# Kernel optimization log

Measured on AMD Instinct MI355X. Metric: run time of the kernel, lower is better.

## Reference

```python
import jax, jax.numpy as jnp
import numpy as np

N_NODES = 50000


def _segment_softmax(alpha, dst, num_segments):
    # alpha: [E, H] edge attention logits, softmax-normalized per destination node
    m = jax.ops.segment_max(alpha, dst, num_segments=num_segments)
    m = jnp.where(jnp.isfinite(m), m, 0.0)
    e = jnp.exp(alpha - m[dst])
    s = jax.ops.segment_sum(e, dst, num_segments=num_segments)
    return e / (s[dst] + 1e-16)


def _gat_layer(x, W, att_src, att_dst, bias, src, dst, heads, ch, concat):
    N = x.shape[0]
    xp = (x @ W).reshape(N, heads, ch)                      # [N, H, C]
    a_s = jnp.einsum('nhc,hc->nh', xp, att_src)              # [N, H]
    a_d = jnp.einsum('nhc,hc->nh', xp, att_dst)              # [N, H]
    alpha = jax.nn.leaky_relu(a_s[src] + a_d[dst], 0.2)      # [E, H]
    alpha = _segment_softmax(alpha, dst, N)
    out = jax.ops.segment_sum(alpha[:, :, None] * xp[src], dst, num_segments=N)  # [N, H, C]
    out = out.reshape(N, heads * ch) if concat else out.mean(axis=1)
    return out + bias


def setup_inputs() -> dict:
    key = jax.random.key(0)
    ks = jax.random.split(key, 10)
    IN, HID, HEADS, OUT, E = 128, 64, 4, 32, 640000
    x = jax.random.normal(ks[0], (N_NODES, IN), jnp.float32)
    edge_index = jax.random.randint(ks[1], (2, E), 0, N_NODES, dtype=jnp.int32)
    W1 = jax.random.normal(ks[2], (IN, HEADS * HID), jnp.float32) * (1.0 / np.sqrt(IN))
    att_src1 = jax.random.normal(ks[3], (HEADS, HID), jnp.float32) * 0.1
    att_dst1 = jax.random.normal(ks[4], (HEADS, HID), jnp.float32) * 0.1
    b1 = jnp.zeros((HEADS * HID,), jnp.float32)
    W2 = jax.random.normal(ks[5], (HEADS * HID, OUT), jnp.float32) * (1.0 / np.sqrt(HEADS * HID))
    att_src2 = jax.random.normal(ks[6], (1, OUT), jnp.float32) * 0.1
    att_dst2 = jax.random.normal(ks[7], (1, OUT), jnp.float32) * 0.1
    b2 = jnp.zeros((OUT,), jnp.float32)
    return {"x": x, "edge_index": edge_index, "W1": W1, "att_src1": att_src1,
            "att_dst1": att_dst1, "b1": b1, "W2": W2, "att_src2": att_src2,
            "att_dst2": att_dst2, "b2": b2}


def reference(x, edge_index, W1, att_src1, att_dst1, b1, W2, att_src2, att_dst2, b2):
    N = x.shape[0]
    # PyG GATConv default: add self-loops
    loop = jnp.arange(N, dtype=edge_index.dtype)
    src = jnp.concatenate([edge_index[0], loop])
    dst = jnp.concatenate([edge_index[1], loop])
    HID = att_src1.shape[1]
    HEADS = att_src1.shape[0]
    OUT = att_src2.shape[1]
    # dropout layers are identity in eval mode
    h = jax.nn.elu(_gat_layer(x, W1, att_src1, att_dst1, b1, src, dst, HEADS, HID, True))
    out = _gat_layer(h, W2, att_src2, att_dst2, b2, src, dst, 1, OUT, False)
    return jax.nn.softmax(out, axis=1)
```

## Files before the change

### kernel.cpp

```cpp
#include <hip/hip_runtime.h>
#include <math.h>
#include <stdint.h>

#define NEG_SENT -1e30f

typedef __attribute__((ext_vector_type(8))) short bf16x8;
typedef __attribute__((ext_vector_type(4))) float f32x4;

__device__ __forceinline__ unsigned short f2bf(float f) {
    unsigned u = __float_as_uint(f);
    unsigned r = u + 0x7FFFu + ((u >> 16) & 1u);
    return (unsigned short)(r >> 16);
}
__device__ __forceinline__ float bf2f(unsigned short h) {
    return __uint_as_float(((unsigned)h) << 16);
}

__global__ __launch_bounds__(256) void transpose_w(const float* __restrict__ w1,
        const float* __restrict__ w2, unsigned short* __restrict__ w1t,
        unsigned short* __restrict__ w2t) {
    int tidx = blockIdx.x * 256 + threadIdx.x;
    if (blockIdx.x < 128) {
        int k = tidx & 127, n = tidx >> 7;
        w1t[tidx] = f2bf(w1[k * 256 + n]);
    } else {
        int idx = tidx - 32768;
        int k = idx & 255, n = idx >> 8;
        w2t[idx] = f2bf(w2[k * 32 + n]);
    }
}

__global__ __launch_bounds__(256) void gemm1_mfma(
        const float* __restrict__ x,
        const unsigned short* __restrict__ w1t,
        const float* __restrict__ att_s, const float* __restrict__ att_d,
        unsigned short* __restrict__ xph,
        float* __restrict__ a_s, float* __restrict__ a_d, int M) {
    int wave = (int)(((long)blockIdx.x * 256 + threadIdx.x) >> 6);
    int lane = threadIdx.x & 63;
    int row0 = wave * 16;
    if (row0 >= M) return;
    int r = lane & 15;
    int g = lane >> 4;
    bf16x8 a[4];
    const float* arow = x + (long)(row0 + r) * 128 + g * 8;
    #pragma unroll
    for (int k0 = 0; k0 < 4; ++k0) {
        float4 f0 = *(const float4*)(arow + k0 * 32);
        float4 f1 = *(const float4*)(arow + k0 * 32 + 4);
        bf16x8 af;
        af[0] = (short)f2bf(f0.x); af[1] = (short)f2bf(f0.y);
        af[2] = (short)f2bf(f0.z); af[3] = (short)f2bf(f0.w);
        af[4] = (short)f2bf(f1.x); af[5] = (short)f2bf(f1.y);
        af[6] = (short)f2bf(f1.z); af[7] = (short)f2bf(f1.w);
        a[k0] = af;
    }
    float as_v[16], ad_v[16];
    #pragma unroll
    for (int nt = 0; nt < 16; ++nt) {
        as_v[nt] = att_s[nt * 16 + r];
        ad_v[nt] = att_d[nt * 16 + r];
    }
    f32x4 acc[16];
    #pragma unroll
    for (int nt = 0; nt < 16; ++nt) acc[nt] = (f32x4){0.f, 0.f, 0.f, 0.f};
    #pragma unroll
    for (int nt = 0; nt < 16; ++nt) {
        const unsigned short* brow = w1t + (long)(nt * 16 + r) * 128 + g * 8;
        #pragma unroll
        for (int k0 = 0; k0 < 4; ++k0) {
            bf16x8 b = *(const bf16x8*)(brow + k0 * 32);
            acc[nt] = __builtin_amdgcn_mfma_f32_16x16x32_bf16(a[k0], b, acc[nt], 0, 0, 0);
        }
    }
    float ps[4][4] = {};
    float pd[4][4] = {};
    #pragma unroll
    for (int nt = 0; nt < 16; ++nt) {
        int hh = nt >> 2;
        #pragma unroll
        for (int q = 0; q < 4; ++q) {
            float v = acc[nt][q];
            xph[(long)(row0 + g * 4 + q) * 256 + nt * 16 + r] = f2bf(v);
            ps[q][hh] += v * as_v[nt];
            pd[q][hh] += v * ad_v[nt];
        }
    }
    #pragma unroll
    for (int off = 1; off < 16; off <<= 1) {
        #pragma unroll
        for (int q = 0; q < 4; ++q)
            #pragma unroll
            for (int hh = 0; hh < 4; ++hh) {
                ps[q][hh] += __shfl_xor(ps[q][hh], off);
                pd[q][hh] += __shfl_xor(pd[q][hh], off);
            }
    }
    if (r == 0) {
        #pragma unroll
        for (int q = 0; q < 4; ++q) {
            int row = row0 + g * 4 + q;
            #pragma unroll
            for (int hh = 0; hh < 4; ++hh) {
                a_s[row * 4 + hh] = ps[q][hh];
                a_d[row * 4 + hh] = pd[q][hh];
            }
        }
    }
}

__global__ __launch_bounds__(256) void gemm2_mfma(
        const unsigned short* __restrict__ hb,
        const unsigned short* __restrict__ w2t,
        const float* __restrict__ att_s, const float* __restrict__ att_d,
        unsigned short* __restrict__ xp2h,
        float* __restrict__ a_s, float* __restrict__ a_d, int M) {
    int wave = (int)(((long)blockIdx.x * 256 + threadIdx.x) >> 6);
    int lane = threadIdx.x & 63;
    int row0 = wave * 16;
    if (row0 >= M) return;
    int r = lane & 15;
    int g = lane >> 4;
    bf16x8 a[8];
    const unsigned short* arow = hb + (long)(row0 + r) * 256 + g * 8;
    #pragma unroll
    for (int k0 = 0; k0 < 8; ++k0)
        a[k0] = *(const bf16x8*)(arow + k0 * 32);
    float as_v[2], ad_v[2];
    #pragma unroll
    for (int nt = 0; nt < 2; ++nt) {
        as_v[nt] = att_s[nt * 16 + r];
        ad_v[nt] = att_d[nt * 16 + r];
    }
    f32x4 acc[2];
    acc[0] = (f32x4){0.f, 0.f, 0.f, 0.f};
    acc[1] = (f32x4){0.f, 0.f, 0.f, 0.f};
    #pragma unroll
    for (int nt = 0; nt < 2; ++nt) {
        const unsigned short* brow = w2t + (long)(nt * 16 + r) * 256 + g * 8;
        #pragma unroll
        for (int k0 = 0; k0 < 8; ++k0) {
            bf16x8 b = *(const bf16x8*)(brow + k0 * 32);
            acc[nt] = __builtin_amdgcn_mfma_f32_16x16x32_bf16(a[k0], b, acc[nt], 0, 0, 0);
        }
    }
    float ps[4] = {}, pd[4] = {};
    #pragma unroll
    for (int nt = 0; nt < 2; ++nt) {
        #pragma unroll
        for (int q = 0; q < 4; ++q) {
            float v = acc[nt][q];
            xp2h[(long)(row0 + g * 4 + q) * 32 + nt * 16 + r] = f2bf(v);
            ps[q] += v * as_v[nt];
            pd[q] += v * ad_v[nt];
        }
    }
    #pragma unroll
    for (int off = 1; off < 16; off <<= 1) {
        #pragma unroll
        for (int q = 0; q < 4; ++q) {
            ps[q] += __shfl_xor(ps[q], off);
            pd[q] += __shfl_xor(pd[q], off);
        }
    }
    if (r == 0) {
        #pragma unroll
        for (int q = 0; q < 4; ++q) {
            a_s[row0 + g * 4 + q] = ps[q];
            a_d[row0 + g * 4 + q] = pd[q];
        }
    }
}

__global__ __launch_bounds__(256) void count_deg(const int* __restrict__ ei,
        int E, int Etot, int* __restrict__ deg) {
    int e = blockIdx.x * 256 + threadIdx.x;
    if (e >= Etot) return;
    int d = (e < E) ? ei[E + e] : e - E;
    atomicAdd(&deg[d], 1);
}

__global__ __launch_bounds__(256) void scan_local(const int* __restrict__ deg,
        int* __restrict__ rowptr, int* __restrict__ blocksum, int N) {
    __shared__ int part[256];
    int b = blockIdx.x, t = threadIdx.x;
    int base = b * 1024 + t * 4;
    int4 v = make_int4(0, 0, 0, 0);
    if (base + 3 < N) {
        v = *(const int4*)(deg + base);
    } else {
        if (base + 0 < N) v.x = deg[base + 0];
        if (base + 1 < N) v.y = deg[base + 1];
        if (base + 2 < N) v.z = deg[base + 2];
        if (base + 3 < N) v.w = deg[base + 3];
    }
    part[t] = v.x + v.y + v.z + v.w;
    __syncthreads();
    #pragma unroll
    for (int off = 1; off < 256; off <<= 1) {
        int val = (t >= off) ? part[t - off] : 0;
        __syncthreads();
        part[t] += val;
        __syncthreads();
    }
    if (t == 255) blocksum[b] = part[255];
    int r0 = (t > 0) ? part[t - 1] : 0;
    int r1 = r0 + v.x;
    int r2 = r1 + v.y;
    int r3 = r2 + v.z;
    if (base + 3 < N) {
        *(int4*)(rowptr + base) = make_int4(r0, r1, r2, r3);
    } else {
        if (base + 0 < N) rowptr[base + 0] = r0;
        if (base + 1 < N) rowptr[base + 1] = r1;
        if (base + 2 < N) rowptr[base + 2] = r2;
        if (base + 3 < N) rowptr[base + 3] = r3;
    }
}

__global__ __launch_bounds__(256) void scan_add(int* __restrict__ rowptr,
        const int* __restrict__ blocksum, int* __restrict__ cursor,
        int N, int Etot, int nb) {
    __shared__ int part[256];
    int b = blockIdx.x, t = threadIdx.x;
    part[t] = (t < nb) ? blocksum[t] : 0;
    __syncthreads();
    #pragma unroll
    for (int off = 1; off < 256; off <<= 1) {
        int val = (t >= off) ? part[t - off] : 0;
        __syncthreads();
        part[t] += val;
        __syncthreads();
    }
    int off_b = (b > 0) ? part[b - 1] : 0;
    int base = b * 1024 + t * 4;
    if (base + 3 < N) {
        int4 v = *(const int4*)(rowptr + base);
        v.x += off_b; v.y += off_b; v.z += off_b; v.w += off_b;
        *(int4*)(rowptr + base) = v;
        *(int4*)(cursor + base) = v;
    } else {
        for (int i = 0; i < 4; ++i) {
            if (base + i < N) {
                int v = rowptr[base + i] + off_b;
                rowptr[base + i] = v;
                cursor[base + i] = v;
            }
        }
    }
    if (b == 0 && t == 0) rowptr[N] = Etot;
}

__global__ __launch_bounds__(256) void scatter_edges(const int* __restrict__ ei,
        int E, int Etot, int* __restrict__ cursor, int* __restrict__ csr_src) {
    int e = blockIdx.x * 256 + threadIdx.x;
    if (e >= Etot) return;
    int s, d;
    if (e < E) { s = ei[e]; d = ei[E + e]; } else { s = e - E; d = s; }
    int pos = atomicAdd(&cursor[d], 1);
    csr_src[pos] = s;
}

__global__ __launch_bounds__(256) void sort_rows(const int* __restrict__ rowptr,
        int* __restrict__ csr_src, int N) {
    __shared__ int buf[4][256];
    __shared__ int mxw[4];
    int t = threadIdx.x;
    int w = t >> 6;
    int lane = t & 63;
    int d = blockIdx.x * 4 + w;
    int row0 = 0, deg = 0;
    if (d < N) { row0 = rowptr[d]; deg = rowptr[d + 1] - row0; }
    int capped = (deg <= 256) ? deg : 0;
    for (int j = lane; j < capped; j += 64) buf[w][j] = csr_src[row0 + j];
    int m = capped;
    #pragma unroll
    for (int off = 32; off; off >>= 1) m = max(m, __shfl_xor(m, off));
    if (lane == 0) mxw[w] = m;
    __syncthreads();
    int itmax = max(max(mxw[0], mxw[1]), max(mxw[2], mxw[3]));
    for (int it = 0; it < itmax; ++it) {
        int start = it & 1;
        #pragma unroll
        for (int rep = 0; rep < 2; ++rep) {
            int k = start + 2 * lane + rep * 128;
            if (k + 1 < capped) {
                int a = buf[w][k], b = buf[w][k + 1];
                if (a > b) { buf[w][k] = b; buf[w][k + 1] = a; }
            }
        }
        __syncthreads();
    }
    for (int j = lane; j < capped; j += 64) csr_src[row0 + j] = buf[w][j];
    if (deg > 256 && lane == 0) {
        for (int i = 1; i < deg; ++i) {
            int key = csr_src[row0 + i];
            int k = i - 1;
            while (k >= 0 && csr_src[row0 + k] > key) {
                csr_src[row0 + k + 1] = csr_src[row0 + k];
                --k;
            }
            csr_src[row0 + k + 1] = key;
        }
    }
}

__device__ __forceinline__ void merge_ms(float& m, float& s, float m2, float s2) {
    float mn = fmaxf(m, m2);
    s = s * expf(m - mn) + s2 * expf(m2 - mn);
    m = mn;
}

__global__ __launch_bounds__(256) void stats_coeff_h4(const int* __restrict__ rowptr,
        const int* __restrict__ csr_src, const float* __restrict__ a_s,
        const float* __restrict__ a_d, unsigned short* __restrict__ coeff, int N) {
    int t = threadIdx.x;
    int d = blockIdx.x * 4 + (t >> 6);
    if (d >= N) return;
    int lane = t & 63;
    int h = lane & 3;
    int j0 = lane >> 2;
    int row0 = rowptr[d];
    int deg = rowptr[d + 1] - row0;
    float ad = a_d[d * 4 + h];
    float m = NEG_SENT, s = 0.f;
    for (int j = j0; j < deg; j += 16) {
        int sn = csr_src[row0 + j];
        float l = a_s[sn * 4 + h] + ad;
        l = l > 0.f ? l : 0.2f * l;
        float mn = fmaxf(m, l);
        s = s * expf(m - mn) + expf(l - mn);
        m = mn;
    }
    #pragma unroll
    for (int off = 4; off <= 32; off <<= 1) {
        float m2 = __shfl_xor(m, off);
        float s2 = __shfl_xor(s, off);
        merge_ms(m, s, m2, s2);
    }
    float inv = 1.f / (s + 1e-16f);
    for (int j = j0; j < deg; j += 16) {
        int sn = csr_src[row0 + j];
        float l = a_s[sn * 4 + h] + ad;
        l = l > 0.f ? l : 0.2f * l;
        coeff[(long)(row0 + j) * 4 + h] = f2bf(expf(l - m) * inv);
    }
}

__global__ __launch_bounds__(256) void agg1_gather_bf16(const int* __restrict__ rowptr,
        const int* __restrict__ csr_src, const unsigned short* __restrict__ coeff,
        const ushort4* __restrict__ xph4, const float* __restrict__ bias,
        ushort4* __restrict__ hb4, int N) {
    int t = threadIdx.x;
    int d = blockIdx.x * 4 + (t >> 6);
    if (d >= N) return;
    int lane = t & 63;
    int hsel = lane >> 4;
    int row0 = rowptr[d];
    int deg = rowptr[d + 1] - row0;
    float4 acc = make_float4(0.f, 0.f, 0.f, 0.f);
    int j = 0;
    for (; j + 4 <= deg; j += 4) {
        long e0 = row0 + j;
        int s0 = csr_src[e0 + 0];
        int s1 = csr_src[e0 + 1];
        int s2 = csr_src[e0 + 2];
        int s3 = csr_src[e0 + 3];
        float c0 = bf2f(coeff[(e0 + 0) * 4 + hsel]);
        float c1 = bf2f(coeff[(e0 + 1) * 4 + hsel]);
        float c2 = bf2f(coeff[(e0 + 2) * 4 + hsel]);
        float c3 = bf2f(coeff[(e0 + 3) * 4 + hsel]);
        ushort4 u0 = xph4[(long)s0 * 64 + lane];
        ushort4 u1 = xph4[(long)s1 * 64 + lane];
        ushort4 u2 = xph4[(long)s2 * 64 + lane];
        ushort4 u3 = xph4[(long)s3 * 64 + lane];
        acc.x += c0 * bf2f(u0.x); acc.y += c0 * bf2f(u0.y);
        acc.z += c0 * bf2f(u0.z); acc.w += c0 * bf2f(u0.w);
        acc.x += c1 * bf2f(u1.x); acc.y += c1 * bf2f(u1.y);
        acc.z += c1 * bf2f(u1.z); acc.w += c1 * bf2f(u1.w);
        acc.x += c2 * bf2f(u2.x); acc.y += c2 * bf2f(u2.y);
        acc.z += c2 * bf2f(u2.z); acc.w += c2 * bf2f(u2.w);
        acc.x += c3 * bf2f(u3.x); acc.y += c3 * bf2f(u3.y);
        acc.z += c3 * bf2f(u3.z); acc.w += c3 * bf2f(u3.w);
    }
    for (; j < deg; ++j) {
        long e = row0 + j;
        int s = csr_src[e];
        float c = bf2f(coeff[e * 4 + hsel]);
        ushort4 u = xph4[(long)s * 64 + lane];
        acc.x += c * bf2f(u.x); acc.y += c * bf2f(u.y);
        acc.z += c * bf2f(u.z); acc.w += c * bf2f(u.w);
    }
    float4 b = ((const float4*)bias)[lane];
    float vx = acc.x + b.x; vx = vx > 0.f ? vx : expm1f(vx);
    float vy = acc.y + b.y; vy = vy > 0.f ? vy : expm1f(vy);
    float vz = acc.z + b.z; vz = vz > 0.f ? vz : expm1f(vz);
    float vw = acc.w + b.w; vw = vw > 0.f ? vw : expm1f(vw);
    ushort4 o;
    o.x = f2bf(vx); o.y = f2bf(vy); o.z = f2bf(vz); o.w = f2bf(vw);
    hb4[(long)d * 64 + lane] = o;
}

__global__ __launch_bounds__(256) void agg2_fused(const int* __restrict__ rowptr,
        const int* __restrict__ csr_src, const float* __restrict__ a_s,
        const float* __restrict__ a_d, const unsigned short* __restrict__ xp2h,
        const float* __restrict__ bias, float* __restrict__ out, int N) {
    int t = threadIdx.x;
    int d = blockIdx.x * 8 + (t >> 5);
    if (d >= N) return;
    int c = t & 31;
    int row0 = rowptr[d];
    int deg = rowptr[d + 1] - row0;
    float ad = a_d[d];
    float m = NEG_SENT, s = 0.f;
    for (int j = c; j < deg; j += 32) {
        int sn = csr_src[row0 + j];
        float l = a_s[sn] + ad;
        l = l > 0.f ? l : 0.2f * l;
        float mn = fmaxf(m, l);
        s = s * expf(m - mn) + expf(l - mn);
        m = mn;
    }
    #pragma unroll
    for (int off = 1; off <= 16; off <<= 1) {
        float m2 = __shfl_xor(m, off, 32);
        float s2 = __shfl_xor(s, off, 32);
        merge_ms(m, s, m2, s2);
    }
    float inv = 1.f / (s + 1e-16f);
    float acc = 0.f;
    int j = 0;
    for (; j + 4 <= deg; j += 4) {
        long e0 = row0 + j;
        int s0 = csr_src[e0 + 0];
        int s1 = csr_src[e0 + 1];
        int s2 = csr_src[e0 + 2];
        int s3 = csr_src[e0 + 3];
        float l0 = a_s[s0] + ad; l0 = l0 > 0.f ? l0 : 0.2f * l0;
        float l1 = a_s[s1] + ad; l1 = l1 > 0.f ? l1 : 0.2f * l1;
        float l2 = a_s[s2] + ad; l2 = l2 > 0.f ? l2 : 0.2f * l2;
        float l3 = a_s[s3] + ad; l3 = l3 > 0.f ? l3 : 0.2f * l3;
        float c0 = expf(l0 - m) * inv;
        float c1 = expf(l1 - m) * inv;
        float c2 = expf(l2 - m) * inv;
        float c3 = expf(l3 - m) * inv;
        float v0 = bf2f(xp2h[(long)s0 * 32 + c]);
        float v1 = bf2f(xp2h[(long)s1 * 32 + c]);
        float v2 = bf2f(xp2h[(long)s2 * 32 + c]);
        float v3 = bf2f(xp2h[(long)s3 * 32 + c]);
        acc += c0 * v0;
        acc += c1 * v1;
        acc += c2 * v2;
        acc += c3 * v3;
    }
    for (; j < deg; ++j) {
        long e = row0 + j;
        int sn = csr_src[e];
        float l = a_s[sn] + ad; l = l > 0.f ? l : 0.2f * l;
        float co = expf(l - m) * inv;
        acc += co * bf2f(xp2h[(long)sn * 32 + c]);
    }
    float v = acc + bias[c];
    float mx = v;
    #pragma unroll
    for (int off = 16; off; off >>= 1) mx = fmaxf(mx, __shfl_xor(mx, off, 32));
    float ex = expf(v - mx);
    float sm = ex;
    #pragma unroll
    for (int off = 16; off; off >>= 1) sm += __shfl_xor(sm, off, 32);
    out[(long)d * 32 + c] = ex / sm;
}

extern "C" void kernel_launch(void* const* d_in, const int* in_sizes, int n_in,
                              void* d_out, int out_size, void* d_ws, size_t ws_size,
                              hipStream_t stream) {
    const float* x   = (const float*)d_in[0];
    const int*   ei  = (const int*)d_in[1];
    const float* W1  = (const float*)d_in[2];
    const float* as1 = (const float*)d_in[3];
    const float* ad1 = (const float*)d_in[4];
    const float* b1  = (const float*)d_in[5];
    const float* W2  = (const float*)d_in[6];
    const float* as2 = (const float*)d_in[7];
    const float* ad2 = (const float*)d_in[8];
    const float* b2  = (const float*)d_in[9];
    float* out = (float*)d_out;

    const int N = in_sizes[0] / 128;
    const int E = in_sizes[1] / 2;
    const int Etot = E + N;

    unsigned short* xp1h = (unsigned short*)d_ws;
    unsigned short* hb   = xp1h + (long)N * 256;
    unsigned short* w1t  = hb + (long)N * 256;
    unsigned short* w2t  = w1t + 32768;
    unsigned short* xp2h = w2t + 8192;
    float* a_s1   = (float*)(xp2h + (long)N * 32);
    float* a_d1   = a_s1 + (long)N * 4;
    float* a_s2   = a_d1 + (long)N * 4;
    float* a_d2   = a_s2 + N;
    unsigned short* coeff1 = (unsigned short*)(a_d2 + N);
    int* deg      = (int*)(coeff1 + (long)Etot * 4);
    int* rowptr   = deg + N;
    int* cursor   = rowptr + N + 4;
    int* csr_src  = cursor + N;
    int* blocksum = csr_src + Etot;

    hipMemsetAsync(deg, 0, (size_t)N * sizeof(int), stream);

    int nbE = (Etot + 255) / 256;
    int nbS = (N + 1023) / 1024;
    count_deg<<<nbE, 256, 0, stream>>>(ei, E, Etot, deg);
    scan_local<<<nbS, 256, 0, stream>>>(deg, rowptr, blocksum, N);
    scan_add<<<nbS, 256, 0, stream>>>(rowptr, blocksum, cursor, N, Etot, nbS);
    scatter_edges<<<nbE, 256, 0, stream>>>(ei, E, Etot, cursor, csr_src);
    sort_rows<<<(N + 3) / 4, 256, 0, stream>>>(rowptr, csr_src, N);

    int gemmBlocks = (((N + 15) / 16) + 3) / 4;
    transpose_w<<<160, 256, 0, stream>>>(W1, W2, w1t, w2t);

    gemm1_mfma<<<gemmBlocks, 256, 0, stream>>>(x, w1t, as1, ad1,
                                               xp1h, a_s1, a_d1, N);
    stats_coeff_h4<<<(N + 3) / 4, 256, 0, stream>>>(rowptr, csr_src, a_s1, a_d1,
                                                    coeff1, N);
    agg1_gather_bf16<<<(N + 3) / 4, 256, 0, stream>>>(rowptr, csr_src, coeff1,
                                              (const ushort4*)xp1h, b1,
                                              (ushort4*)hb, N);

    gemm2_mfma<<<gemmBlocks, 256, 0, stream>>>(hb, w2t, as2, ad2,
                                               xp2h, a_s2, a_d2, N);
    agg2_fused<<<(N + 7) / 8, 256, 0, stream>>>(rowptr, csr_src, a_s2, a_d2,
                                                xp2h, b2, out, N);
}
```

Baseline: 274.2 us.

## Fuse softmax stats with layer-1 aggregation via LDS coefficients; merge weight prep into degree count

Merges the layer-1 softmax-statistics kernel and the gather-aggregation kernel into one. Per-edge attention coefficients for up to 256 edges per node are staged in shared memory rather than written to and re-read from a global coeff buffer. Edges past 256 have their coefficient recomputed inline. The weight transpose/bf16 conversion is also folded into the degree-count kernel as extra blocks, removing one launch. The trade-off is a block-wide sync that couples four waves and 8KB of LDS per block, which may reduce occupancy.

After: 258.3 us. -5.8%, faster.

```diff
diff --git a/kernel.cpp b/kernel.cpp
--- a/kernel.cpp
+++ b/kernel.cpp
@@ -16,17 +16,26 @@
     return __uint_as_float(((unsigned)h) << 16);
 }
 
-__global__ __launch_bounds__(256) void transpose_w(const float* __restrict__ w1,
+__global__ __launch_bounds__(256) void prep_count(const float* __restrict__ w1,
         const float* __restrict__ w2, unsigned short* __restrict__ w1t,
-        unsigned short* __restrict__ w2t) {
-    int tidx = blockIdx.x * 256 + threadIdx.x;
-    if (blockIdx.x < 128) {
-        int k = tidx & 127, n = tidx >> 7;
-        w1t[tidx] = f2bf(w1[k * 256 + n]);
+        unsigned short* __restrict__ w2t, const int* __restrict__ ei,
+        int E, int Etot, int* __restrict__ deg) {
+    int b = blockIdx.x;
+    if (b < 160) {
+        int tidx = b * 256 + threadIdx.x;
+        if (b < 128) {
+            int k = tidx & 127, n = tidx >> 7;
+            w1t[tidx] = f2bf(w1[k * 256 + n]);
+        } else {
+            int idx = tidx - 32768;
+            int k = idx & 255, n = idx >> 8;
+            w2t[idx] = f2bf(w2[k * 32 + n]);
+        }
     } else {
-        int idx = tidx - 32768;
-        int k = idx & 255, n = idx >> 8;
-        w2t[idx] = f2bf(w2[k * 32 + n]);
+        int e = (b - 160) * 256 + threadIdx.x;
+        if (e >= Etot) return;
+        int d = (e < E) ? ei[E + e] : e - E;
+        atomicAdd(&deg[d], 1);
     }
 }
 
@@ -172,14 +181,6 @@
     }
 }
 
-__global__ __launch_bounds__(256) void count_deg(const int* __restrict__ ei,
-        int E, int Etot, int* __restrict__ deg) {
-    int e = blockIdx.x * 256 + threadIdx.x;
-    if (e >= Etot) return;
-    int d = (e < E) ? ei[E + e] : e - E;
-    atomicAdd(&deg[d], 1);
-}
-
 __global__ __launch_bounds__(256) void scan_local(const int* __restrict__ deg,
         int* __restrict__ rowptr, int* __restrict__ blocksum, int N) {
     __shared__ int part[256];
@@ -311,18 +312,21 @@
     m = mn;
 }
 
-__global__ __launch_bounds__(256) void stats_coeff_h4(const int* __restrict__ rowptr,
+__global__ __launch_bounds__(256) void agg1_fused(const int* __restrict__ rowptr,
         const int* __restrict__ csr_src, const float* __restrict__ a_s,
-        const float* __restrict__ a_d, unsigned short* __restrict__ coeff, int N) {
+        const float* __restrict__ a_d, const ushort4* __restrict__ xph4,
+        const float* __restrict__ bias, ushort4* __restrict__ hb4, int N) {
+    __shared__ unsigned short cbuf[4][1024];
     int t = threadIdx.x;
-    int d = blockIdx.x * 4 + (t >> 6);
-    if (d >= N) return;
+    int w = t >> 6;
     int lane = t & 63;
+    int d = blockIdx.x * 4 + w;
+    bool active = d < N;
+    int row0 = 0, deg = 0;
+    if (active) { row0 = rowptr[d]; deg = rowptr[d + 1] - row0; }
     int h = lane & 3;
     int j0 = lane >> 2;
-    int row0 = rowptr[d];
-    int deg = rowptr[d + 1] - row0;
-    float ad = a_d[d * 4 + h];
+    float ad = active ? a_d[d * 4 + h] : 0.f;
     float m = NEG_SENT, s = 0.f;
     for (int j = j0; j < deg; j += 16) {
         int sn = csr_src[row0 + j];
@@ -339,37 +343,31 @@
         merge_ms(m, s, m2, s2);
     }
     float inv = 1.f / (s + 1e-16f);
-    for (int j = j0; j < deg; j += 16) {
+    int cap = deg < 256 ? deg : 256;
+    for (int j = j0; j < cap; j += 16) {
         int sn = csr_src[row0 + j];
         float l = a_s[sn * 4 + h] + ad;
         l = l > 0.f ? l : 0.2f * l;
-        coeff[(long)(row0 + j) * 4 + h] = f2bf(expf(l - m) * inv);
-    }
-}
-
-__global__ __launch_bounds__(256) void agg1_gather_bf16(const int* __restrict__ rowptr,
-        const int* __restrict__ csr_src, const unsigned short* __restrict__ coeff,
-        const ushort4* __restrict__ xph4, const float* __restrict__ bias,
-        ushort4* __restrict__ hb4, int N) {
-    int t = threadIdx.x;
-    int d = blockIdx.x * 4 + (t >> 6);
-    if (d >= N) return;
-    int lane = t & 63;
+        cbuf[w][j * 4 + h] = f2bf(expf(l - m) * inv);
+    }
+    __syncthreads();
+    if (!active) return;
     int hsel = lane >> 4;
-    int row0 = rowptr[d];
-    int deg = rowptr[d + 1] - row0;
+    float m_h   = __shfl(m, hsel);
+    float inv_h = __shfl(inv, hsel);
+    float ad_h  = __shfl(ad, hsel);
     float4 acc = make_float4(0.f, 0.f, 0.f, 0.f);
     int j = 0;
-    for (; j + 4 <= deg; j += 4) {
+    for (; j + 4 <= cap; j += 4) {
         long e0 = row0 + j;
         int s0 = csr_src[e0 + 0];
         int s1 = csr_src[e0 + 1];
         int s2 = csr_src[e0 + 2];
         int s3 = csr_src[e0 + 3];
-        float c0 = bf2f(coeff[(e0 + 0) * 4 + hsel]);
-        float c1 = bf2f(coeff[(e0 + 1) * 4 + hsel]);
-        float c2 = bf2f(coeff[(e0 + 2) * 4 + hsel]);
-        float c3 = bf2f(coeff[(e0 + 3) * 4 + hsel]);
+        float c0 = bf2f(cbuf[w][(j + 0) * 4 + hsel]);
+        float c1 = bf2f(cbuf[w][(j + 1) * 4 + hsel]);
+        float c2 = bf2f(cbuf[w][(j + 2) * 4 + hsel]);
+        float c3 = bf2f(cbuf[w][(j + 3) * 4 + hsel]);
         ushort4 u0 = xph4[(long)s0 * 64 + lane];
         ushort4 u1 = xph4[(long)s1 * 64 + lane];
         ushort4 u2 = xph4[(long)s2 * 64 + lane];
@@ -385,9 +383,16 @@
     }
     for (; j < deg; ++j) {
         long e = row0 + j;
-        int s = csr_src[e];
-        float c = bf2f(coeff[e * 4 + hsel]);
-        ushort4 u = xph4[(long)s * 64 + lane];
+        int sn = csr_src[e];
+        float c;
+        if (j < 256) {
+            c = bf2f(cbuf[w][j * 4 + hsel]);
+        } else {
+            float l = a_s[sn * 4 + hsel] + ad_h;
+            l = l > 0.f ? l : 0.2f * l;
+            c = bf2f(f2bf(expf(l - m_h) * inv_h));
+        }
+        ushort4 u = xph4[(long)sn * 64 + lane];
         acc.x += c * bf2f(u.x); acc.y += c * bf2f(u.y);
         acc.z += c * bf2f(u.z); acc.w += c * bf2f(u.w);
     }
@@ -499,8 +504,7 @@
     float* a_d1   = a_s1 + (long)N * 4;
     float* a_s2   = a_d1 + (long)N * 4;
     float* a_d2   = a_s2 + N;
-    unsigned short* coeff1 = (unsigned short*)(a_d2 + N);
-    int* deg      = (int*)(coeff1 + (long)Etot * 4);
+    int* deg      = (int*)(a_d2 + N);
     int* rowptr   = deg + N;
     int* cursor   = rowptr + N + 4;
     int* csr_src  = cursor + N;
@@ -510,22 +514,19 @@
 
     int nbE = (Etot + 255) / 256;
     int nbS = (N + 1023) / 1024;
-    count_deg<<<nbE, 256, 0, stream>>>(ei, E, Etot, deg);
+    prep_count<<<160 + nbE, 256, 0, stream>>>(W1, W2, w1t, w2t, ei, E, Etot, deg);
     scan_local<<<nbS, 256, 0, stream>>>(deg, rowptr, blocksum, N);
     scan_add<<<nbS, 256, 0, stream>>>(rowptr, blocksum, cursor, N, Etot, nbS);
     scatter_edges<<<nbE, 256, 0, stream>>>(ei, E, Etot, cursor, csr_src);
     sort_rows<<<(N + 3) / 4, 256, 0, stream>>>(rowptr, csr_src, N);
 
     int gemmBlocks = (((N + 15) / 16) + 3) / 4;
-    transpose_w<<<160, 256, 0, stream>>>(W1, W2, w1t, w2t);
 
     gemm1_mfma<<<gemmBlocks, 256, 0, stream>>>(x, w1t, as1, ad1,
                                                xp1h, a_s1, a_d1, N);
-    stats_coeff_h4<<<(N + 3) / 4, 256, 0, stream>>>(rowptr, csr_src, a_s1, a_d1,
-                                                    coeff1, N);
-    agg1_gather_bf16<<<(N + 3) / 4, 256, 0, stream>>>(rowptr, csr_src, coeff1,
-                                              (const ushort4*)xp1h, b1,
-                                              (ushort4*)hb, N);
+    agg1_fused<<<(N + 3) / 4, 256, 0, stream>>>(rowptr, csr_src, a_s1, a_d1,
+                                                (const ushort4*)xp1h, b1,
+                                                (ushort4*)hb, N);
 
     gemm2_mfma<<<gemmBlocks, 256, 0, stream>>>(hb, w2t, as2, ad2,
                                                xp2h, a_s2, a_d2, N);
```
